# Kernel tuning notes

Hardware: AMD Instinct MI355X
Metric: run time of the kernel (lower is better)

## Reference

```python
import jax, jax.numpy as jnp
import numpy as np

DIM = 1024
HEADS = 16
HEAD_DIM = DIM // HEADS
SCALE = HEAD_DIM ** -0.5
B, N = 2, 2048


def setup_inputs() -> dict:
    key = jax.random.key(0)
    ks = jax.random.split(key, 12)
    s = DIM ** -0.5
    return {
        "x_real": jax.random.normal(ks[0], (B, N, DIM), jnp.float32),
        "x_imag": jax.random.normal(ks[1], (B, N, DIM), jnp.float32),
        "Wqkv_r": jax.random.normal(ks[2], (3 * DIM, DIM), jnp.float32) * s,
        "bqkv_r": jax.random.normal(ks[3], (3 * DIM,), jnp.float32) * 0.01,
        "Wqkv_i": jax.random.normal(ks[4], (3 * DIM, DIM), jnp.float32) * s,
        "bqkv_i": jax.random.normal(ks[5], (3 * DIM,), jnp.float32) * 0.01,
        "Wout_r": jax.random.normal(ks[6], (DIM, DIM), jnp.float32) * s,
        "bout_r": jax.random.normal(ks[7], (DIM,), jnp.float32) * 0.01,
        "Wout_i": jax.random.normal(ks[8], (DIM, DIM), jnp.float32) * s,
        "bout_i": jax.random.normal(ks[9], (DIM,), jnp.float32) * 0.01,
    }


def _split_heads(qkv):
    # (B, N, 3*D) -> q, k, v each (B, H, N, hd)
    b, n, _ = qkv.shape
    qkv = qkv.reshape(b, n, 3, HEADS, HEAD_DIM).transpose(2, 0, 3, 1, 4)
    return qkv[0], qkv[1], qkv[2]


def reference(x_real, x_imag, Wqkv_r, bqkv_r, Wqkv_i, bqkv_i,
              Wout_r, bout_r, Wout_i, bout_i):
    b, n, d = x_real.shape
    q_r, k_r, v_r = _split_heads(x_real @ Wqkv_r.T + bqkv_r)
    q_i, k_i, v_i = _split_heads(x_imag @ Wqkv_i.T + bqkv_i)

    # complex score: (q_r + i q_i) (k_r - i k_i)^T pattern per source
    attn_real = (jnp.einsum('bhqd,bhkd->bhqk', q_r, k_r)
                 + jnp.einsum('bhqd,bhkd->bhqk', q_i, k_i)) * SCALE
    attn_imag = (jnp.einsum('bhqd,bhkd->bhqk', q_i, k_r)
                 - jnp.einsum('bhqd,bhkd->bhqk', q_r, k_i)) * SCALE
    attn_mag = jnp.sqrt(attn_real ** 2 + attn_imag ** 2)
    w = jax.nn.softmax(attn_mag, axis=-1)

    out_r = jnp.einsum('bhqk,bhkd->bhqd', w, v_r).transpose(0, 2, 1, 3).reshape(b, n, d)
    out_i = jnp.einsum('bhqk,bhkd->bhqd', w, v_i).transpose(0, 2, 1, 3).reshape(b, n, d)
    out_r = out_r @ Wout_r.T + bout_r
    out_i = out_i @ Wout_i.T + bout_i
    return out_r, out_i
```

## Files before the change

kernel.cpp:

```cpp
#include <hip/hip_runtime.h>


#define DIM_   1024
#define HEADS_ 16
#define HD_    64
#define BB_    2
#define NN_    2048
#define MTOT_  (BB_*NN_)
#define SCALE_ 0.125f

typedef __bf16 bf16;
typedef __bf16 bf16x8 __attribute__((ext_vector_type(8)));
typedef short  s16x8  __attribute__((ext_vector_type(8)));
typedef float  fx4    __attribute__((ext_vector_type(4)));

__device__ __forceinline__ bf16x8 neg8(bf16x8 v) {
    s16x8 s;
    __builtin_memcpy(&s, &v, sizeof(s));
    s ^= (short)0x8000;
    bf16x8 r;
    __builtin_memcpy(&r, &s, sizeof(r));
    return r;
}

__device__ __forceinline__ void gl_lds16(const void* g, void* l) {
    __builtin_amdgcn_global_load_lds(
        (const __attribute__((address_space(1))) unsigned int*)g,
        (__attribute__((address_space(3))) unsigned int*)l, 16, 0, 0);
}

__global__ __launch_bounds__(256) void cvt_prepass(
    const float* __restrict__ xr, const float* __restrict__ xi,
    const float* __restrict__ wqr, const float* __restrict__ wqi,
    const float* __restrict__ wor, const float* __restrict__ woi,
    bf16* __restrict__ xbf, bf16* __restrict__ wqkv, bf16* __restrict__ wout)
{
    const int bid = blockIdx.x;
    const float* src; bf16* dst; int rel;
    if      (bid < 2048) { src = xr;  dst = xbf;           rel = bid; }
    else if (bid < 4096) { src = xi;  dst = xbf + 4194304; rel = bid - 2048; }
    else if (bid < 5632) { src = wqr; dst = wqkv;          rel = bid - 4096; }
    else if (bid < 7168) { src = wqi; dst = wqkv + 3145728; rel = bid - 5632; }
    else if (bid < 7680) { src = wor; dst = wout;          rel = bid - 7168; }
    else                 { src = woi; dst = wout + 1048576; rel = bid - 7680; }
    size_t base = (size_t)rel * 2048 + (size_t)threadIdx.x * 8;
    fx4 a = *(const fx4*)(src + base);
    fx4 b = *(const fx4*)(src + base + 4);
    bf16x8 o;
#pragma unroll
    for (int j = 0; j < 4; ++j) { o[j] = (bf16)a[j]; o[j+4] = (bf16)b[j]; }
    *(bf16x8*)(dst + base) = o;
}

#define GEMM_CORE(Aptr, Bptr)                                                  \
    __shared__ __align__(16) bf16 As[128*64];                                  \
    __shared__ __align__(16) bf16 Bs[128*64];                                  \
    const int tid  = threadIdx.x;                                              \
    const int w    = tid >> 6, lane = tid & 63;                                \
    const int quad = lane >> 4, lc = lane & 15;                                \
    const int wm   = (w >> 1) * 64, wn = (w & 1) * 64;                         \
    const int rj   = lane >> 3;                                                \
    const int sc   = (lane & 7) ^ rj;                                          \
    const fx4 fzero = {0.f, 0.f, 0.f, 0.f};                                    \
    fx4 acc[4][4];                                                             \
    _Pragma("unroll")                                                          \
    for (int mi = 0; mi < 4; ++mi)                                             \
        _Pragma("unroll")                                                      \
        for (int ni = 0; ni < 4; ++ni) acc[mi][ni] = fzero;                    \
    for (int k0 = 0; k0 < DIM_; k0 += 64) {                                    \
        _Pragma("unroll")                                                      \
        for (int j = 0; j < 4; ++j) {                                          \
            int grp = j*4 + w;                                                 \
            int gr  = grp*8 + rj;                                              \
            gl_lds16(Aptr + (size_t)(m0+gr)*DIM_ + k0 + sc*8, As + grp*512);   \
            gl_lds16(Bptr + (size_t)(n0+gr)*DIM_ + k0 + sc*8, Bs + grp*512);   \
        }                                                                      \
        __syncthreads();                                                       \
        bf16x8 af[2][4], bfr[2][4];                                            \
        _Pragma("unroll")                                                      \
        for (int ks = 0; ks < 2; ++ks) {                                       \
            _Pragma("unroll")                                                  \
            for (int mi = 0; mi < 4; ++mi)                                     \
                af[ks][mi] = *(bf16x8*)&As[(wm+mi*16+lc)*64 + (((ks*4+quad)^(lc&7))*8)]; \
            _Pragma("unroll")                                                  \
            for (int ni = 0; ni < 4; ++ni)                                     \
                bfr[ks][ni] = *(bf16x8*)&Bs[(wn+ni*16+lc)*64 + (((ks*4+quad)^(lc&7))*8)]; \
        }                                                                      \
        _Pragma("unroll")                                                      \
        for (int ks = 0; ks < 2; ++ks)                                         \
            _Pragma("unroll")                                                  \
            for (int mi = 0; mi < 4; ++mi)                                     \
                _Pragma("unroll")                                              \
                for (int ni = 0; ni < 4; ++ni)                                 \
                    acc[mi][ni] = __builtin_amdgcn_mfma_f32_16x16x32_bf16(     \
                        af[ks][mi], bfr[ks][ni], acc[mi][ni], 0, 0, 0);        \
        __syncthreads();                                                       \
    }

__global__ __launch_bounds__(256) void qkv_gemm_dma(
    const bf16* __restrict__ xbf, const bf16* __restrict__ wqkv,
    const float* __restrict__ br, const float* __restrict__ bi,
    bf16* __restrict__ qbuf, bf16* __restrict__ kbuf, bf16* __restrict__ vbuf)
{
    const int z = blockIdx.z;
    const bf16* __restrict__ Ap = xbf  + (size_t)z * 4194304;
    const bf16* __restrict__ Bp = wqkv + (size_t)z * 3145728;
    const float* __restrict__ bias = z ? bi : br;
    const int n0 = blockIdx.x * 128;
    const int m0 = blockIdx.y * 128;

    GEMM_CORE(Ap, Bp)

#pragma unroll
    for (int mi = 0; mi < 4; ++mi)
#pragma unroll
        for (int ni = 0; ni < 4; ++ni)
#pragma unroll
            for (int r = 0; r < 4; ++r) {
                int gm = m0 + wm + mi*16 + quad*4 + r;
                int gc = n0 + wn + ni*16 + lc;
                float val = acc[mi][ni][r] + bias[gc];
                bf16 bv = (bf16)val;
                int which = gc >> 10, h = (gc >> 6) & 15, hd = gc & 63;
                int b = gm >> 11, n = gm & 2047;
                size_t base = (size_t)((z*BB_ + b)*HEADS_ + h);
                if (which == 0)      qbuf[(base*NN_ + n)*HD_ + hd] = bv;
                else if (which == 1) kbuf[(base*NN_ + n)*HD_ + hd] = bv;
                else                 vbuf[(base*HD_ + hd)*NN_ + n] = bv;
            }
}

__global__ __launch_bounds__(256) void out_gemm_dma(
    const bf16* __restrict__ obuf, const bf16* __restrict__ wout,
    const float* __restrict__ br, const float* __restrict__ bi,
    float* __restrict__ out)
{
    const int z = blockIdx.z;
    const bf16* __restrict__ Ap = obuf + (size_t)z * 4194304;
    const bf16* __restrict__ Bp = wout + (size_t)z * 1048576;
    const float* __restrict__ bias = z ? bi : br;
    float* __restrict__ dst = out + (size_t)z * 4194304;
    const int n0 = blockIdx.x * 128;
    const int m0 = blockIdx.y * 128;

    GEMM_CORE(Ap, Bp)

#pragma unroll
    for (int mi = 0; mi < 4; ++mi)
#pragma unroll
        for (int ni = 0; ni < 4; ++ni)
#pragma unroll
            for (int r = 0; r < 4; ++r) {
                int gm = m0 + wm + mi*16 + quad*4 + r;
                int gc = n0 + wn + ni*16 + lc;
                dst[(size_t)gm*DIM_ + gc] = acc[mi][ni][r] + bias[gc];
            }
}

#define KT 32
#define NSTEP (NN_/KT)

__global__ __launch_bounds__(256, 4) void attn_fwd(
    const bf16* __restrict__ qbuf, const bf16* __restrict__ kbuf,
    const bf16* __restrict__ vbuf, bf16* __restrict__ obuf)
{
    const int bid = blockIdx.x;
    const int xcd = bid & 7;
    const int loc = bid >> 3;
    const int hb  = xcd*4 + (loc >> 5);
    const int blk = loc & 31;
    const int b = hb >> 4, h = hb & 15;

    const int tid  = threadIdx.x;
    const int w    = tid >> 6, lane = tid & 63;
    const int quad = lane >> 4, lc = lane & 15;
    const int q0   = blk*64 + w*16;

    __shared__ __align__(16) bf16 KV[2*8192];
    __shared__ __align__(16) bf16 Ps[4*16*40];
    bf16* psw = Ps + w*(16*40);

    const size_t hR = (size_t)(b)*HEADS_ + h;
    const size_t hI = (size_t)(BB_ + b)*HEADS_ + h;
    const bf16* qrg = qbuf + hR*NN_*HD_;
    const bf16* qig = qbuf + hI*NN_*HD_;
    const char* krg = (const char*)(kbuf + hR*NN_*HD_);
    const char* kig = (const char*)(kbuf + hI*NN_*HD_);
    const char* vrg = (const char*)(vbuf + hR*HD_*NN_);
    const char* vig = (const char*)(vbuf + hI*HD_*NN_);

    const bf16* pr = qrg + (size_t)(q0 + lc)*HD_ + quad*8;
    const bf16* pi = qig + (size_t)(q0 + lc)*HD_ + quad*8;
    bf16x8 qr0 = *(const bf16x8*)(pr);
    bf16x8 qr1 = *(const bf16x8*)(pr + 32);
    bf16x8 qi0 = *(const bf16x8*)(pi);
    bf16x8 qi1 = *(const bf16x8*)(pi + 32);
    bf16x8 nqr0 = neg8(qr0), nqr1 = neg8(qr1);

    const char* stg_base;
    size_t lane_off, step_mul, j_mul;
    if (w < 2) {
        stg_base = w ? kig : krg;
        lane_off = (size_t)(lane >> 3)*128 + (size_t)((lane & 7) ^ (lane >> 3))*16;
        step_mul = (size_t)KT * 128;
        j_mul    = 1024;
    } else {
        stg_base = (w == 3) ? vig : vrg;
        lane_off = (size_t)(lane >> 2)*4096 + (size_t)((lane & 3) ^ ((lane >> 3) & 3))*16;
        step_mul = (size_t)KT * 2;
        j_mul    = 65536;
    }
    bf16* lds_arr = KV + w*2048;

    const fx4 fzero = {0.f, 0.f, 0.f, 0.f};
    fx4 O[2][4];
    float l_[4];
#pragma unroll
    for (int r = 0; r < 4; ++r) l_[r] = 0.f;
#pragma unroll
    for (int ri = 0; ri < 2; ++ri)
#pragma unroll
        for (int vb = 0; vb < 4; ++vb) O[ri][vb] = fzero;
    bf16x8 pf;
    bf16x8 vf[2][4];

    const float CEXP = SCALE_ * 1.44269504f;

    {
        const char* g = stg_base + lane_off;
#pragma unroll
        for (int j = 0; j < 4; ++j)
            gl_lds16(g + j*j_mul, lds_arr + j*512);
    }
    __syncthreads();

    for (int s = 0; s < NSTEP; ++s) {
        const int buf = s & 1;
        bf16* kvb = KV + buf*8192;

        if (s < NSTEP-1) {
            const char* g = stg_base + (size_t)(s+1)*step_mul + lane_off;
            bf16* l = lds_arr + (buf ^ 1)*8192;
#pragma unroll
            for (int j = 0; j < 4; ++j)
                gl_lds16(g + j*j_mul, l + j*512);
        }

        if (s > 0) {
#pragma unroll
            for (int ri = 0; ri < 2; ++ri)
#pragma unroll
                for (int vb = 0; vb < 4; ++vb)
                    O[ri][vb] = __builtin_amdgcn_mfma_f32_16x16x32_bf16(
                        pf, vf[ri][vb], O[ri][vb], 0, 0, 0);
        }

#pragma unroll
        for (int kb = 0; kb < 2; ++kb) {
            int r = kb*16 + lc;
            int c0 = quad ^ (r & 7);
            int c1 = (4 + quad) ^ (r & 7);
            bf16x8 kr0f = *(bf16x8*)&kvb[0*2048 + r*64 + c0*8];
            bf16x8 kr1f = *(bf16x8*)&kvb[0*2048 + r*64 + c1*8];
            bf16x8 ki0f = *(bf16x8*)&kvb[1*2048 + r*64 + c0*8];
            bf16x8 ki1f = *(bf16x8*)&kvb[1*2048 + r*64 + c1*8];
            fx4 sr = fzero, si = fzero;
            sr = __builtin_amdgcn_mfma_f32_16x16x32_bf16(qr0,  kr0f, sr, 0,0,0);
            sr = __builtin_amdgcn_mfma_f32_16x16x32_bf16(qr1,  kr1f, sr, 0,0,0);
            sr = __builtin_amdgcn_mfma_f32_16x16x32_bf16(qi0,  ki0f, sr, 0,0,0);
            sr = __builtin_amdgcn_mfma_f32_16x16x32_bf16(qi1,  ki1f, sr, 0,0,0);
            si = __builtin_amdgcn_mfma_f32_16x16x32_bf16(qi0,  kr0f, si, 0,0,0);
            si = __builtin_amdgcn_mfma_f32_16x16x32_bf16(qi1,  kr1f, si, 0,0,0);
            si = __builtin_amdgcn_mfma_f32_16x16x32_bf16(nqr0, ki0f, si, 0,0,0);
            si = __builtin_amdgcn_mfma_f32_16x16x32_bf16(nqr1, ki1f, si, 0,0,0);
#pragma unroll
            for (int r4 = 0; r4 < 4; ++r4) {
                float s2 = sr[r4]*sr[r4] + si[r4]*si[r4];
                float mg = __builtin_amdgcn_sqrtf(s2);
                float pv = __builtin_amdgcn_exp2f(mg * CEXP);
                l_[r4] += pv;
                psw[(quad*4 + r4)*40 + kb*16 + lc] = (bf16)pv;
            }
        }

        pf = *(bf16x8*)&psw[lc*40 + quad*8];
#pragma unroll
        for (int ri = 0; ri < 2; ++ri)
#pragma unroll
            for (int vb = 0; vb < 4; ++vb) {
                int r = vb*16 + lc;
                int c = quad ^ ((r >> 1) & 3);
                vf[ri][vb] = *(bf16x8*)&kvb[(2+ri)*2048 + r*32 + c*8];
            }

        __syncthreads();
    }

#pragma unroll
    for (int ri = 0; ri < 2; ++ri)
#pragma unroll
        for (int vb = 0; vb < 4; ++vb)
            O[ri][vb] = __builtin_amdgcn_mfma_f32_16x16x32_bf16(
                pf, vf[ri][vb], O[ri][vb], 0, 0, 0);

#pragma unroll
    for (int off = 1; off < 16; off <<= 1)
#pragma unroll
        for (int r = 0; r < 4; ++r)
            l_[r] += __shfl_xor(l_[r], off);
    float inv[4];
#pragma unroll
    for (int r = 0; r < 4; ++r) inv[r] = 1.f / l_[r];

    bf16* obr = obuf + ((size_t)(b)*NN_)*DIM_;
    bf16* obi = obuf + ((size_t)(BB_ + b)*NN_)*DIM_;
#pragma unroll
    for (int vb = 0; vb < 4; ++vb)
#pragma unroll
        for (int r = 0; r < 4; ++r) {
            int gn = q0 + quad*4 + r;
            int gc = h*HD_ + vb*16 + lc;
            obr[(size_t)gn*DIM_ + gc] = (bf16)(O[0][vb][r] * inv[r]);
            obi[(size_t)gn*DIM_ + gc] = (bf16)(O[1][vb][r] * inv[r]);
        }
}

__global__ __launch_bounds__(256) void qkv_gemm_legacy(
    const float* __restrict__ xr, const float* __restrict__ xi,
    const float* __restrict__ Wr, const float* __restrict__ Wi,
    const float* __restrict__ br, const float* __restrict__ bi,
    bf16* __restrict__ qbuf, bf16* __restrict__ kbuf, bf16* __restrict__ vbuf)
{
    const int z = blockIdx.z;
    const float* __restrict__ A    = z ? xi : xr;
    const float* __restrict__ W    = z ? Wi : Wr;
    const float* __restrict__ bias = z ? bi : br;
    const int n0 = blockIdx.x * 128;
    const int m0 = blockIdx.y * 128;

    __shared__ bf16 As[128*40];
    __shared__ bf16 Bs[128*40];

    const int tid  = threadIdx.x;
    const int w    = tid >> 6, lane = tid & 63;
    const int quad = lane >> 4, lc = lane & 15;
    const int wm   = (w >> 1) * 64, wn = (w & 1) * 64;

    const fx4 fzero = {0.f, 0.f, 0.f, 0.f};
    fx4 acc[4][4];
#pragma unroll
    for (int mi = 0; mi < 4; ++mi)
#pragma unroll
        for (int ni = 0; ni < 4; ++ni) acc[mi][ni] = fzero;

    for (int k0 = 0; k0 < DIM_; k0 += 32) {
#pragma unroll
        for (int it = 0; it < 2; ++it) {
            int flat = it*2048 + tid*8;
            int row = flat >> 5, col = flat & 31;
            const float* pa = A + (size_t)(m0+row)*DIM_ + k0 + col;
            const float* pb = W + (size_t)(n0+row)*DIM_ + k0 + col;
            fx4 a0 = *(const fx4*)pa, a1 = *(const fx4*)(pa+4);
            fx4 b0 = *(const fx4*)pb, b1 = *(const fx4*)(pb+4);
            bf16x8 av, bv;
#pragma unroll
            for (int j = 0; j < 4; ++j) {
                av[j] = (bf16)a0[j]; av[j+4] = (bf16)a1[j];
                bv[j] = (bf16)b0[j]; bv[j+4] = (bf16)b1[j];
            }
            *(bf16x8*)&As[row*40 + col] = av;
            *(bf16x8*)&Bs[row*40 + col] = bv;
        }
        __syncthreads();

        bf16x8 af[4], bfr[4];
#pragma unroll
        for (int mi = 0; mi < 4; ++mi) af[mi]  = *(bf16x8*)&As[(wm + mi*16 + lc)*40 + quad*8];
#pragma unroll
        for (int ni = 0; ni < 4; ++ni) bfr[ni] = *(bf16x8*)&Bs[(wn + ni*16 + lc)*40 + quad*8];
#pragma unroll
        for (int mi = 0; mi < 4; ++mi)
#pragma unroll
            for (int ni = 0; ni < 4; ++ni)
                acc[mi][ni] = __builtin_amdgcn_mfma_f32_16x16x32_bf16(af[mi], bfr[ni], acc[mi][ni], 0, 0, 0);
        __syncthreads();
    }

#pragma unroll
    for (int mi = 0; mi < 4; ++mi)
#pragma unroll
        for (int ni = 0; ni < 4; ++ni)
#pragma unroll
            for (int r = 0; r < 4; ++r) {
                int gm = m0 + wm + mi*16 + quad*4 + r;
                int gc = n0 + wn + ni*16 + lc;
                float val = acc[mi][ni][r] + bias[gc];
                bf16 bv = (bf16)val;
                int which = gc >> 10, h = (gc >> 6) & 15, hd = gc & 63;
                int b = gm >> 11, n = gm & 2047;
                size_t base = (size_t)((z*BB_ + b)*HEADS_ + h);
                if (which == 0)      qbuf[(base*NN_ + n)*HD_ + hd] = bv;
                else if (which == 1) kbuf[(base*NN_ + n)*HD_ + hd] = bv;
                else                 vbuf[(base*HD_ + hd)*NN_ + n] = bv;
            }
}

__global__ __launch_bounds__(256) void out_gemm_legacy(
    const bf16* __restrict__ obuf,
    const float* __restrict__ Wr, const float* __restrict__ Wi,
    const float* __restrict__ br, const float* __restrict__ bi,
    float* __restrict__ out)
{
    const int z = blockIdx.z;
    const bf16*  __restrict__ A    = obuf + (size_t)z * MTOT_ * DIM_;
    const float* __restrict__ W    = z ? Wi : Wr;
    const float* __restrict__ bias = z ? bi : br;
    float* __restrict__ dst        = out + (size_t)z * MTOT_ * DIM_;
    const int n0 = blockIdx.x * 128;
    const int m0 = blockIdx.y * 128;

    __shared__ bf16 As[128*40];
    __shared__ bf16 Bs[128*40];

    const int tid  = threadIdx.x;
    const int w    = tid >> 6, lane = tid & 63;
    const int quad = lane >> 4, lc = lane & 15;
    const int wm   = (w >> 1) * 64, wn = (w & 1) * 64;

    const fx4 fzero = {0.f, 0.f, 0.f, 0.f};
    fx4 acc[4][4];
#pragma unroll
    for (int mi = 0; mi < 4; ++mi)
#pragma unroll
        for (int ni = 0; ni < 4; ++ni) acc[mi][ni] = fzero;

    for (int k0 = 0; k0 < DIM_; k0 += 32) {
#pragma unroll
        for (int it = 0; it < 2; ++it) {
            int flat = it*2048 + tid*8;
            int row = flat >> 5, col = flat & 31;
            *(bf16x8*)&As[row*40 + col] = *(const bf16x8*)(A + (size_t)(m0+row)*DIM_ + k0 + col);
            const float* pb = W + (size_t)(n0+row)*DIM_ + k0 + col;
            fx4 b0 = *(const fx4*)pb, b1 = *(const fx4*)(pb+4);
            bf16x8 bv;
#pragma unroll
            for (int j = 0; j < 4; ++j) { bv[j] = (bf16)b0[j]; bv[j+4] = (bf16)b1[j]; }
            *(bf16x8*)&Bs[row*40 + col] = bv;
        }
        __syncthreads();

        bf16x8 af[4], bfr[4];
#pragma unroll
        for (int mi = 0; mi < 4; ++mi) af[mi]  = *(bf16x8*)&As[(wm + mi*16 + lc)*40 + quad*8];
#pragma unroll
        for (int ni = 0; ni < 4; ++ni) bfr[ni] = *(bf16x8*)&Bs[(wn + ni*16 + lc)*40 + quad*8];
#pragma unroll
        for (int mi = 0; mi < 4; ++mi)
#pragma unroll
            for (int ni = 0; ni < 4; ++ni)
                acc[mi][ni] = __builtin_amdgcn_mfma_f32_16x16x32_bf16(af[mi], bfr[ni], acc[mi][ni], 0, 0, 0);
        __syncthreads();
    }

#pragma unroll
    for (int mi = 0; mi < 4; ++mi)
#pragma unroll
        for (int ni = 0; ni < 4; ++ni)
#pragma unroll
            for (int r = 0; r < 4; ++r) {
                int gm = m0 + wm + mi*16 + quad*4 + r;
                int gc = n0 + wn + ni*16 + lc;
                dst[(size_t)gm*DIM_ + gc] = acc[mi][ni][r] + bias[gc];
            }
}

extern "C" void kernel_launch(void* const* d_in, const int* in_sizes, int n_in,
                              void* d_out, int out_size, void* d_ws, size_t ws_size,
                              hipStream_t stream) {
    const float* xr  = (const float*)d_in[0];
    const float* xi  = (const float*)d_in[1];
    const float* Wqr = (const float*)d_in[2];
    const float* bqr = (const float*)d_in[3];
    const float* Wqi = (const float*)d_in[4];
    const float* bqi = (const float*)d_in[5];
    const float* Wor = (const float*)d_in[6];
    const float* bor = (const float*)d_in[7];
    const float* Woi = (const float*)d_in[8];
    const float* boi = (const float*)d_in[9];
    float* out = (float*)d_out;

    bf16* ws = (bf16*)d_ws;
    const size_t NEED = 83886080ull;

    if (ws_size >= NEED) {
        bf16* xbf  = ws;
        bf16* wqkv = ws + 8388608;
        bf16* wout = ws + 14680064;
        bf16* qb   = ws + 16777216;
        bf16* kb   = ws + 25165824;
        bf16* vb   = ws + 33554432;
        bf16* obuf = xbf;

        cvt_prepass<<<dim3(8192), 256, 0, stream>>>(xr, xi, Wqr, Wqi, Wor, Woi,
                                                    xbf, wqkv, wout);
        qkv_gemm_dma<<<dim3(24, 32, 2), 256, 0, stream>>>(xbf, wqkv, bqr, bqi,
                                                          qb, kb, vb);
        attn_fwd<<<dim3(1024), 256, 0, stream>>>(qb, kb, vb, obuf);
        out_gemm_dma<<<dim3(8, 32, 2), 256, 0, stream>>>(obuf, wout, bor, boi, out);
    } else {
        const size_t per = (size_t)2 * BB_ * HEADS_ * NN_ * HD_;
        bf16* qb   = ws;
        bf16* kb   = ws + per;
        bf16* vb   = ws + 2*per;
        bf16* obuf = ws + 3*per;
        qkv_gemm_legacy<<<dim3(24, 32, 2), 256, 0, stream>>>(xr, xi, Wqr, Wqi,
                                                             bqr, bqi, qb, kb, vb);
        attn_fwd<<<dim3(1024), 256, 0, stream>>>(qb, kb, vb, obuf);
        out_gemm_legacy<<<dim3(8, 32, 2), 256, 0, stream>>>(obuf, Wor, Woi,
                                                            bor, boi, out);
    }
}
```

Measured before the change: 365.9 us.

## Triple-buffer attention K/V tiles with 8-wave blocks and partial vmcnt barrier

The attention kernel now uses 512-thread blocks covering 128 queries each, so every staged K/V tile is shared by twice as many waves. Staging moves from a double to a triple LDS buffer with a two-step prefetch distance. A raw s_waitcnt vmcnt(2) plus s_barrier replaces __syncthreads, so the next tile's loads can stay in flight across the barrier. LDS offsets are precomputed, and K fragments are loaded before the MFMAs. In exchange, LDS use per block rises and there are half as many blocks, which may lower occupancy and latency hiding. The hand-written waitcnt also depends on the compiler not reordering the async LDS loads.

```diff
diff --git a/kernel.cpp b/kernel.cpp
--- a/kernel.cpp
+++ b/kernel.cpp
@@ -28,6 +28,8 @@
         (const __attribute__((address_space(1))) unsigned int*)g,
         (__attribute__((address_space(3))) unsigned int*)l, 16, 0, 0);
 }
+
+#define PIPE_SYNC() asm volatile("s_waitcnt vmcnt(2)\n\ts_barrier" ::: "memory")
 
 __global__ __launch_bounds__(256) void cvt_prepass(
     const float* __restrict__ xr, const float* __restrict__ xi,
@@ -160,25 +162,25 @@
 #define KT 32
 #define NSTEP (NN_/KT)
 
-__global__ __launch_bounds__(256, 4) void attn_fwd(
+__global__ __launch_bounds__(512, 4) void attn_fwd(
     const bf16* __restrict__ qbuf, const bf16* __restrict__ kbuf,
     const bf16* __restrict__ vbuf, bf16* __restrict__ obuf)
 {
     const int bid = blockIdx.x;
     const int xcd = bid & 7;
     const int loc = bid >> 3;
-    const int hb  = xcd*4 + (loc >> 5);
-    const int blk = loc & 31;
+    const int hb  = xcd*4 + (loc >> 4);
+    const int blk = loc & 15;
     const int b = hb >> 4, h = hb & 15;
 
     const int tid  = threadIdx.x;
     const int w    = tid >> 6, lane = tid & 63;
     const int quad = lane >> 4, lc = lane & 15;
-    const int q0   = blk*64 + w*16;
-
-    __shared__ __align__(16) bf16 KV[2*8192];
-    __shared__ __align__(16) bf16 Ps[4*16*40];
-    bf16* psw = Ps + w*(16*40);
+    const int q0   = blk*128 + w*16;
+
+    __shared__ __align__(16) bf16 KV[3*8192];
+    __shared__ __align__(16) bf16 Ps[8*16*40];
+    bf16* psw = Ps + w*640;
 
     const size_t hR = (size_t)(b)*HEADS_ + h;
     const size_t hI = (size_t)(BB_ + b)*HEADS_ + h;
@@ -197,20 +199,33 @@
     bf16x8 qi1 = *(const bf16x8*)(pi + 32);
     bf16x8 nqr0 = neg8(qr0), nqr1 = neg8(qr1);
 
-    const char* stg_base;
+    const int arr = w >> 1, half = w & 1;
+    const char* stg_base = (arr == 0) ? krg : (arr == 1) ? kig
+                         : (arr == 2) ? vrg : vig;
     size_t lane_off, step_mul, j_mul;
-    if (w < 2) {
-        stg_base = w ? kig : krg;
+    if (arr < 2) {
         lane_off = (size_t)(lane >> 3)*128 + (size_t)((lane & 7) ^ (lane >> 3))*16;
-        step_mul = (size_t)KT * 128;
-        j_mul    = 1024;
+        step_mul = 4096;  j_mul = 1024;
     } else {
-        stg_base = (w == 3) ? vig : vrg;
         lane_off = (size_t)(lane >> 2)*4096 + (size_t)((lane & 3) ^ ((lane >> 3) & 3))*16;
-        step_mul = (size_t)KT * 2;
-        j_mul    = 65536;
-    }
-    bf16* lds_arr = KV + w*2048;
+        step_mul = 64;    j_mul = 65536;
+    }
+    const char* stg0 = stg_base + (size_t)half*2*j_mul + lane_off;
+    const int lds_base = arr*2048 + half*1024;
+
+    int koff[2][2], voff[4];
+#pragma unroll
+    for (int kb = 0; kb < 2; ++kb)
+#pragma unroll
+        for (int hf = 0; hf < 2; ++hf) {
+            int r = kb*16 + lc;
+            koff[kb][hf] = r*64 + (((hf*4 + quad) ^ (r & 7))*8);
+        }
+#pragma unroll
+    for (int vb = 0; vb < 4; ++vb) {
+        int r = vb*16 + lc;
+        voff[vb] = r*32 + ((quad ^ ((r >> 1) & 3))*8);
+    }
 
     const fx4 fzero = {0.f, 0.f, 0.f, 0.f};
     fx4 O[2][4];
@@ -227,23 +242,22 @@
     const float CEXP = SCALE_ * 1.44269504f;
 
     {
-        const char* g = stg_base + lane_off;
-#pragma unroll
-        for (int j = 0; j < 4; ++j)
-            gl_lds16(g + j*j_mul, lds_arr + j*512);
-    }
-    __syncthreads();
-
+        bf16* l = KV + lds_base;
+        gl_lds16(stg0,          l);
+        gl_lds16(stg0 + j_mul,  l + 512);
+        l = KV + 8192 + lds_base;
+        gl_lds16(stg0 + step_mul,         l);
+        gl_lds16(stg0 + step_mul + j_mul, l + 512);
+    }
+    PIPE_SYNC();
+
+    int b0 = 0, b1 = 8192, b2 = 16384;
     for (int s = 0; s < NSTEP; ++s) {
-        const int buf = s & 1;
-        bf16* kvb = KV + buf*8192;
-
-        if (s < NSTEP-1) {
-            const char* g = stg_base + (size_t)(s+1)*step_mul + lane_off;
-            bf16* l = lds_arr + (buf ^ 1)*8192;
-#pragma unroll
-            for (int j = 0; j < 4; ++j)
-                gl_lds16(g + j*j_mul, l + j*512);
+        if (s < NSTEP-2) {
+            const char* g = stg0 + (size_t)(s+2)*step_mul;
+            bf16* l = KV + b2 + lds_base;
+            gl_lds16(g,         l);
+            gl_lds16(g + j_mul, l + 512);
         }
 
         if (s > 0) {
@@ -255,24 +269,26 @@
                         pf, vf[ri][vb], O[ri][vb], 0, 0, 0);
         }
 
+        bf16x8 kr_[2][2], ki_[2][2];
+#pragma unroll
+        for (int kb = 0; kb < 2; ++kb)
+#pragma unroll
+            for (int hf = 0; hf < 2; ++hf) {
+                kr_[kb][hf] = *(bf16x8*)&KV[b0 + koff[kb][hf]];
+                ki_[kb][hf] = *(bf16x8*)&KV[b0 + 2048 + koff[kb][hf]];
+            }
+
 #pragma unroll
         for (int kb = 0; kb < 2; ++kb) {
-            int r = kb*16 + lc;
-            int c0 = quad ^ (r & 7);
-            int c1 = (4 + quad) ^ (r & 7);
-            bf16x8 kr0f = *(bf16x8*)&kvb[0*2048 + r*64 + c0*8];
-            bf16x8 kr1f = *(bf16x8*)&kvb[0*2048 + r*64 + c1*8];
-            bf16x8 ki0f = *(bf16x8*)&kvb[1*2048 + r*64 + c0*8];
-            bf16x8 ki1f = *(bf16x8*)&kvb[1*2048 + r*64 + c1*8];
             fx4 sr = fzero, si = fzero;
-            sr = __builtin_amdgcn_mfma_f32_16x16x32_bf16(qr0,  kr0f, sr, 0,0,0);
-            sr = __builtin_amdgcn_mfma_f32_16x16x32_bf16(qr1,  kr1f, sr, 0,0,0);
-            sr = __builtin_amdgcn_mfma_f32_16x16x32_bf16(qi0,  ki0f, sr, 0,0,0);
-            sr = __builtin_amdgcn_mfma_f32_16x16x32_bf16(qi1,  ki1f, sr, 0,0,0);
-            si = __builtin_amdgcn_mfma_f32_16x16x32_bf16(qi0,  kr0f, si, 0,0,0);
-            si = __builtin_amdgcn_mfma_f32_16x16x32_bf16(qi1,  kr1f, si, 0,0,0);
-            si = __builtin_amdgcn_mfma_f32_16x16x32_bf16(nqr0, ki0f, si, 0,0,0);
-            si = __builtin_amdgcn_mfma_f32_16x16x32_bf16(nqr1, ki1f, si, 0,0,0);
+            sr = __builtin_amdgcn_mfma_f32_16x16x32_bf16(qr0,  kr_[kb][0], sr, 0,0,0);
+            sr = __builtin_amdgcn_mfma_f32_16x16x32_bf16(qr1,  kr_[kb][1], sr, 0,0,0);
+            sr = __builtin_amdgcn_mfma_f32_16x16x32_bf16(qi0,  ki_[kb][0], sr, 0,0,0);
+            sr = __builtin_amdgcn_mfma_f32_16x16x32_bf16(qi1,  ki_[kb][1], sr, 0,0,0);
+            si = __builtin_amdgcn_mfma_f32_16x16x32_bf16(qi0,  kr_[kb][0], si, 0,0,0);
+            si = __builtin_amdgcn_mfma_f32_16x16x32_bf16(qi1,  kr_[kb][1], si, 0,0,0);
+            si = __builtin_amdgcn_mfma_f32_16x16x32_bf16(nqr0, ki_[kb][0], si, 0,0,0);
+            si = __builtin_amdgcn_mfma_f32_16x16x32_bf16(nqr1, ki_[kb][1], si, 0,0,0);
 #pragma unroll
             for (int r4 = 0; r4 < 4; ++r4) {
                 float s2 = sr[r4]*sr[r4] + si[r4]*si[r4];
@@ -287,13 +303,11 @@
 #pragma unroll
         for (int ri = 0; ri < 2; ++ri)
 #pragma unroll
-            for (int vb = 0; vb < 4; ++vb) {
-                int r = vb*16 + lc;
-                int c = quad ^ ((r >> 1) & 3);
-                vf[ri][vb] = *(bf16x8*)&kvb[(2+ri)*2048 + r*32 + c*8];
-            }
-
-        __syncthreads();
+            for (int vb = 0; vb < 4; ++vb)
+                vf[ri][vb] = *(bf16x8*)&KV[b0 + (2+ri)*2048 + voff[vb]];
+
+        PIPE_SYNC();
+        int t = b0; b0 = b1; b1 = b2; b2 = t;
     }
 
 #pragma unroll
@@ -505,7 +519,7 @@
                                                     xbf, wqkv, wout);
         qkv_gemm_dma<<<dim3(24, 32, 2), 256, 0, stream>>>(xbf, wqkv, bqr, bqi,
                                                           qb, kb, vb);
-        attn_fwd<<<dim3(1024), 256, 0, stream>>>(qb, kb, vb, obuf);
+        attn_fwd<<<dim3(512), 512, 0, stream>>>(qb, kb, vb, obuf);
         out_gemm_dma<<<dim3(8, 32, 2), 256, 0, stream>>>(obuf, wout, bor, boi, out);
     } else {
         const size_t per = (size_t)2 * BB_ * HEADS_ * NN_ * HD_;
@@ -515,7 +529,7 @@
         bf16* obuf = ws + 3*per;
         qkv_gemm_legacy<<<dim3(24, 32, 2), 256, 0, stream>>>(xr, xi, Wqr, Wqi,
                                                              bqr, bqi, qb, kb, vb);
-        attn_fwd<<<dim3(1024), 256, 0, stream>>>(qb, kb, vb, obuf);
+        attn_fwd<<<dim3(512), 512, 0, stream>>>(qb, kb, vb, obuf);
         out_gemm_legacy<<<dim3(8, 32, 2), 256, 0, stream>>>(obuf, Wor, Woi,
                                                             bor, boi, out);
     }
```

Result: faster. 347.0 us (-5.2%).
